# Kernel optimization log

Measured on AMD Instinct MI355X. Metric: run time of the kernel, lower is better.

The kernel has to match this reference:

```python
import jax, jax.numpy as jnp
import numpy as np

COMMITMENT_COST = 0.25


def setup_inputs() -> dict:
    key = jax.random.key(0)
    k1, k2 = jax.random.split(key)
    z_e = jax.random.normal(k1, (32, 256, 32, 32), dtype=jnp.float32)
    codebook = jax.random.normal(k2, (1024, 256), dtype=jnp.float32)
    return {"z_e": z_e, "codebook": codebook}


def reference(z_e, codebook):
    B, D, H, W = z_e.shape
    # (B, D, H, W) -> (N, D), N = B*H*W
    z_flat = jnp.transpose(z_e, (0, 2, 3, 1)).reshape(-1, D)
    # squared L2 distances to every codebook entry: (N, K)
    distances = (
        jnp.sum(z_flat * z_flat, axis=1, keepdims=True)
        - 2.0 * (z_flat @ codebook.T)
        + jnp.sum(codebook * codebook, axis=1)
    )
    codes = jnp.argmin(distances, axis=1)          # (N,)
    z_q = jnp.transpose(codebook[codes].reshape(B, H, W, D), (0, 3, 1, 2))
    # straight-through estimator
    z_q_st = z_e + jax.lax.stop_gradient(z_q - z_e)
    codebook_loss = jnp.mean((jax.lax.stop_gradient(z_q) - z_e) ** 2)
    commitment_loss = jnp.mean((z_q - jax.lax.stop_gradient(z_e)) ** 2)
    vq_loss = codebook_loss + COMMITMENT_COST * commitment_loss
    indices = codes.reshape(B, H, W)
    return z_q_st, indices, vq_loss
```

## Files before the change

kernel.cpp:

```cpp
#include <hip/hip_runtime.h>
#include <cstdint>
#include <cstddef>


typedef __attribute__((ext_vector_type(8))) short bf16x8;
typedef __attribute__((ext_vector_type(4))) float f32x4;

#define GL2LDS(g, l) __builtin_amdgcn_global_load_lds( \
    (__attribute__((address_space(1))) const void*)(g), \
    (__attribute__((address_space(3))) void*)(l), 16, 0, 0)

__device__ __forceinline__ unsigned short rne_bf16(float f) {
    unsigned u = __float_as_uint(f);
    return (unsigned short)((u + 0x7FFFu + ((u >> 16) & 1u)) >> 16);
}
__device__ __forceinline__ float bf16_to_f(unsigned short h) {
    return __uint_as_float((unsigned)h << 16);
}

__global__ __launch_bounds__(256)
void vq_cnorm_kernel(const float* __restrict__ cb, float* __restrict__ cnorm)
{
    const int k = blockIdx.x * 256 + threadIdx.x;
    const float4* row = reinterpret_cast<const float4*>(cb + (size_t)k * 256);
    float s0 = 0.f, s1 = 0.f, s2 = 0.f, s3 = 0.f;
#pragma unroll 8
    for (int i = 0; i < 64; ++i) {
        float4 v = row[i];
        s0 = fmaf(v.x, v.x, s0);
        s1 = fmaf(v.y, v.y, s1);
        s2 = fmaf(v.z, v.z, s2);
        s3 = fmaf(v.w, v.w, s3);
    }
    cnorm[k] = (s0 + s1) + (s2 + s3);
}

__global__ __launch_bounds__(256)
void vq_csplit_kernel(const float* __restrict__ cb, unsigned short* __restrict__ c0,
                      unsigned short* __restrict__ c1, unsigned short* __restrict__ c2)
{
    const int idx = blockIdx.x * 256 + threadIdx.x;
    float4 v = reinterpret_cast<const float4*>(cb)[idx];
    float f[4] = { v.x, v.y, v.z, v.w };
    ushort4 h0, h1, h2;
    unsigned short* p0[4] = { &h0.x, &h0.y, &h0.z, &h0.w };
    unsigned short* p1[4] = { &h1.x, &h1.y, &h1.z, &h1.w };
    unsigned short* p2[4] = { &h2.x, &h2.y, &h2.z, &h2.w };
#pragma unroll
    for (int j = 0; j < 4; ++j) {
        unsigned short b0 = rne_bf16(f[j]); float r1 = f[j] - bf16_to_f(b0);
        unsigned short b1 = rne_bf16(r1);   float r2 = r1 - bf16_to_f(b1);
        unsigned short b2 = rne_bf16(r2);
        *p0[j] = b0; *p1[j] = b1; *p2[j] = b2;
    }
    reinterpret_cast<ushort4*>(c0)[idx] = h0;
    reinterpret_cast<ushort4*>(c1)[idx] = h1;
    reinterpret_cast<ushort4*>(c2)[idx] = h2;
}

__global__ __launch_bounds__(256)
void vq_zsplit_kernel(const float* __restrict__ z, unsigned short* __restrict__ z0,
                      unsigned short* __restrict__ z1, unsigned short* __restrict__ z2)
{
    __shared__ float zl[64 * 264];
    const int t = threadIdx.x, blk = blockIdx.x;
    const int b = blk >> 4, hw0 = (blk & 15) << 6;
    const float* zb = z + ((size_t)b << 18) + hw0;
#pragma unroll 8
    for (int i = 0; i < 64; ++i) {
        int idx = i * 256 + t;
        int d = idx >> 6, hwl = idx & 63;
        zl[hwl * 264 + d] = zb[(size_t)d * 1024 + hwl];
    }
    __syncthreads();
    const int n0 = (b << 10) + hw0;
#pragma unroll
    for (int p = 0; p < 8; ++p) {
        const int hwl = p * 8 + (t >> 5);
        const int d0 = (t & 31) * 8;
        const float* src = &zl[hwl * 264 + d0];
        unsigned short h0[8], h1[8], h2[8];
#pragma unroll
        for (int j = 0; j < 8; ++j) {
            float f = src[j];
            unsigned short b0 = rne_bf16(f);  float r1 = f - bf16_to_f(b0);
            unsigned short b1 = rne_bf16(r1); float r2 = r1 - bf16_to_f(b1);
            unsigned short b2 = rne_bf16(r2);
            h0[j] = b0; h1[j] = b1; h2[j] = b2;
        }
        const size_t o = (size_t)(n0 + hwl) * 256 + d0;
        ushort4 a;
        a = ushort4{h0[0],h0[1],h0[2],h0[3]}; *reinterpret_cast<ushort4*>(z0 + o)     = a;
        a = ushort4{h0[4],h0[5],h0[6],h0[7]}; *reinterpret_cast<ushort4*>(z0 + o + 4) = a;
        a = ushort4{h1[0],h1[1],h1[2],h1[3]}; *reinterpret_cast<ushort4*>(z1 + o)     = a;
        a = ushort4{h1[4],h1[5],h1[6],h1[7]}; *reinterpret_cast<ushort4*>(z1 + o + 4) = a;
        a = ushort4{h2[0],h2[1],h2[2],h2[3]}; *reinterpret_cast<ushort4*>(z2 + o)     = a;
        a = ushort4{h2[4],h2[5],h2[6],h2[7]}; *reinterpret_cast<ushort4*>(z2 + o + 4) = a;
    }
}

__global__ __launch_bounds__(256)
void vq_mfma_argmin_kernel(const unsigned short* __restrict__ zp,
                           const unsigned short* __restrict__ cp,
                           const float* __restrict__ cnorm,
                           unsigned long long* __restrict__ packed)
{
    __shared__ unsigned short At[128 * 64];
    __shared__ unsigned short Bt[128 * 64];

    const int t = threadIdx.x, l = t & 63, w = t >> 6;
    const int wr = w >> 1, wc = w & 1;
    const int nid = ((blockIdx.x & 7) << 8) | (blockIdx.x >> 3);
    const int bm = nid >> 3, bn = nid & 7;
    const int arow = bm * 128, brow = bn * 128;

    const unsigned short* zparts[3] = { zp, zp + 8388608u, zp + 16777216u };
    const unsigned short* cparts[3] = { cp, cp + 262144u,  cp + 524288u };

    f32x4 acc[4][4];
#pragma unroll
    for (int m = 0; m < 4; ++m)
#pragma unroll
        for (int n = 0; n < 4; ++n) acc[m][n] = f32x4{0.f, 0.f, 0.f, 0.f};

    const int srow = w * 8 + (l >> 3);
    const int scol = (((l & 7) ^ ((l >> 3) & 7))) * 8;

    const int lo16 = l & 15, hi4 = l >> 4, l7 = l & 7;
    const int coff0 = ((hi4    ) ^ l7) * 8;
    const int coff1 = ((hi4 + 4) ^ l7) * 8;
    const unsigned short* Arow = &At[(wr * 64 + lo16) * 64];
    const unsigned short* Brow = &Bt[(wc * 64 + lo16) * 64];

    const int ASEG[6] = { 0, 1, 2, 0, 1, 0 };
    const int BSEG[6] = { 0, 0, 0, 1, 1, 2 };

#pragma unroll
    for (int seg = 0; seg < 6; ++seg) {
        const unsigned short* As = zparts[ASEG[seg]];
        const unsigned short* Bs = cparts[BSEG[seg]];
#pragma unroll
        for (int k4 = 0; k4 < 4; ++k4) {
            const int ko = k4 * 64;
            __syncthreads();
#pragma unroll
            for (int i = 0; i < 4; ++i) {
                GL2LDS(As + (size_t)(arow + i * 32 + srow) * 256 + ko + scol,
                       &At[(i * 32 + w * 8) * 64]);
                GL2LDS(Bs + (size_t)(brow + i * 32 + srow) * 256 + ko + scol,
                       &Bt[(i * 32 + w * 8) * 64]);
            }
            __syncthreads();
#pragma unroll
            for (int kk = 0; kk < 2; ++kk) {
                const int co = kk ? coff1 : coff0;
                bf16x8 a[4], b[4];
#pragma unroll
                for (int m = 0; m < 4; ++m)
                    a[m] = *reinterpret_cast<const bf16x8*>(Arow + m * 16 * 64 + co);
#pragma unroll
                for (int n = 0; n < 4; ++n)
                    b[n] = *reinterpret_cast<const bf16x8*>(Brow + n * 16 * 64 + co);
#pragma unroll
                for (int m = 0; m < 4; ++m)
#pragma unroll
                    for (int n = 0; n < 4; ++n)
                        acc[m][n] = __builtin_amdgcn_mfma_f32_16x16x32_bf16(
                            a[m], b[n], acc[m][n], 0, 0, 0);
            }
        }
    }

    int coln[4]; float cnv[4];
#pragma unroll
    for (int n = 0; n < 4; ++n) {
        coln[n] = brow + wc * 64 + n * 16 + (l & 15);
        cnv[n] = cnorm[coln[n]];
    }
#pragma unroll
    for (int m = 0; m < 4; ++m) {
#pragma unroll
        for (int j = 0; j < 4; ++j) {
            unsigned long long best = 0xFFFFFFFFFFFFFFFFull;
#pragma unroll
            for (int n = 0; n < 4; ++n) {
                float d = fmaf(-2.0f, acc[m][n][j], cnv[n]);
                unsigned u = __float_as_uint(d);
                u = (u & 0x80000000u) ? ~u : (u | 0x80000000u);
                unsigned long long pk = ((unsigned long long)u << 32) | (unsigned)coln[n];
                best = pk < best ? pk : best;
            }
#pragma unroll
            for (int mask = 1; mask <= 8; mask <<= 1) {
                unsigned long long o = __shfl_xor(best, mask, 64);
                best = o < best ? o : best;
            }
            if ((l & 15) == 0) {
                const int row = arow + wr * 64 + m * 16 + (l >> 4) * 4 + j;
                atomicMin(&packed[row], best);
            }
        }
    }
}

__global__ __launch_bounds__(256, 2)
void vq_gather_packed_kernel(const float* __restrict__ cb, const float* __restrict__ z,
                             const unsigned long long* __restrict__ packed,
                             float* __restrict__ out_zq, float* __restrict__ out_idx,
                             float* __restrict__ loss)
{
    __shared__ float rows[64 * 257];
    __shared__ int   ks[64];
    __shared__ float wsum[4];

    const int t   = threadIdx.x;
    const int blk = blockIdx.x;
    const int b   = blk >> 4;
    const int hw0 = (blk & 15) << 6;
    const int n0  = blk << 6;

    if (t < 64) {
        const int k = (int)(packed[n0 + t] & 0xFFFFFFFFull);
        ks[t] = k;
        out_idx[n0 + t] = (float)k;
    }
    __syncthreads();

#pragma unroll 4
    for (int i = 0; i < 64; ++i) {
        rows[i * 257 + t] = cb[(size_t)ks[i] * 256 + t];
    }
    __syncthreads();

    const int dq = t >> 6;
    const int hw = t & 63;
    const size_t obase = ((size_t)b << 18) + hw0 + hw;
    float sum = 0.f;
#pragma unroll 4
    for (int dd = 0; dd < 64; ++dd) {
        const int d = (dq << 6) + dd;
        const float  q  = rows[hw * 257 + d];
        const size_t a  = obase + (size_t)d * 1024;
        const float  zv = z[a];
        out_zq[a] = q;
        const float diff = q - zv;
        sum = fmaf(diff, diff, sum);
    }
#pragma unroll
    for (int m = 1; m <= 32; m <<= 1) sum += __shfl_xor(sum, m, 64);
    if ((t & 63) == 0) wsum[t >> 6] = sum;
    __syncthreads();
    if (t == 0) {
        const float s = (wsum[0] + wsum[1]) + (wsum[2] + wsum[3]);
        atomicAdd(loss, s * (1.25f / 8388608.0f));
    }
}

__global__ __launch_bounds__(256)
void vq_transpose_kernel(const float* __restrict__ cb, float* __restrict__ ctT)
{
    __shared__ float tile[64 * 65];
    const int t  = threadIdx.x;
    const int kb = blockIdx.x >> 2, db = blockIdx.x & 3;
    const int k0 = kb << 6, d0 = db << 6;
#pragma unroll
    for (int i = 0; i < 16; ++i) {
        int idx = i * 256 + t;
        int r = idx >> 6, c = idx & 63;
        tile[r * 65 + c] = cb[(size_t)(k0 + r) * 256 + d0 + c];
    }
    __syncthreads();
#pragma unroll
    for (int i = 0; i < 16; ++i) {
        int idx = i * 256 + t;
        int r = idx >> 6, c = idx & 63;
        ctT[(size_t)(d0 + r) * 1024 + k0 + c] = tile[c * 65 + r];
    }
}

__global__ __launch_bounds__(512, 2)
void vq_argmin_kernel(const float* __restrict__ z, const float* __restrict__ ctT,
                      const float* __restrict__ cnorm, int* __restrict__ codes,
                      float* __restrict__ out_idx)
{
    __shared__ float zt[256 * 64];
    __shared__ float ct[16 * 256];
    const int t = threadIdx.x, tx = t & 63, ty = t >> 6, p0 = ty << 3;
    const int blk = blockIdx.x, b = blk >> 4, hw0 = (blk & 15) << 6;
    const float* zbase = z + ((size_t)b << 18) + hw0;
#pragma unroll
    for (int i = 0; i < 8; ++i) {
        int idx = i * 512 + t;
        int d = idx >> 4, c4 = (idx & 15) << 2;
        float4 v = *reinterpret_cast<const float4*>(zbase + (size_t)d * 1024 + c4);
        *reinterpret_cast<float4*>(&zt[d * 64 + c4]) = v;
    }
    float minv[8]; int mini[8];
#pragma unroll
    for (int i = 0; i < 8; ++i) { minv[i] = 3.0e38f; mini[i] = 0; }
    const float* zrd = &zt[p0];
    const float* crd = &ct[tx << 2];
    for (int kt = 0; kt < 4; ++kt) {
        const int k0 = kt << 8;
        float acc[8][4];
#pragma unroll
        for (int i = 0; i < 8; ++i)
#pragma unroll
            for (int j = 0; j < 4; ++j) acc[i][j] = 0.f;
        for (int dc = 0; dc < 16; ++dc) {
            const int d0 = dc << 4;
            __syncthreads();
#pragma unroll
            for (int i = 0; i < 2; ++i) {
                int idx = i * 512 + t;
                int r = idx >> 6, c4 = (idx & 63) << 2;
                float4 v = *reinterpret_cast<const float4*>(ctT + (size_t)(d0 + r) * 1024 + k0 + c4);
                *reinterpret_cast<float4*>(&ct[r * 256 + c4]) = v;
            }
            __syncthreads();
            const float* zp = zrd + d0 * 64;
#pragma unroll
            for (int d = 0; d < 16; ++d) {
                float4 za = *reinterpret_cast<const float4*>(zp + d * 64);
                float4 zb = *reinterpret_cast<const float4*>(zp + d * 64 + 4);
                float4 cc = *reinterpret_cast<const float4*>(crd + d * 256);
#define VQ_FMA_ROW(ii, zv)                          \
                acc[ii][0] = fmaf(zv, cc.x, acc[ii][0]); \
                acc[ii][1] = fmaf(zv, cc.y, acc[ii][1]); \
                acc[ii][2] = fmaf(zv, cc.z, acc[ii][2]); \
                acc[ii][3] = fmaf(zv, cc.w, acc[ii][3]);
                VQ_FMA_ROW(0, za.x) VQ_FMA_ROW(1, za.y) VQ_FMA_ROW(2, za.z) VQ_FMA_ROW(3, za.w)
                VQ_FMA_ROW(4, zb.x) VQ_FMA_ROW(5, zb.y) VQ_FMA_ROW(6, zb.z) VQ_FMA_ROW(7, zb.w)
#undef VQ_FMA_ROW
            }
        }
#pragma unroll
        for (int j = 0; j < 4; ++j) {
            const int k = k0 + (tx << 2) + j;
            const float cn = cnorm[k];
#pragma unroll
            for (int i = 0; i < 8; ++i) {
                float dist = fmaf(-2.0f, acc[i][j], cn);
                if (dist < minv[i]) { minv[i] = dist; mini[i] = k; }
            }
        }
    }
#pragma unroll
    for (int m = 1; m <= 32; m <<= 1) {
#pragma unroll
        for (int i = 0; i < 8; ++i) {
            float ov = __shfl_xor(minv[i], m, 64);
            int   oi = __shfl_xor(mini[i], m, 64);
            if (ov < minv[i] || (ov == minv[i] && oi < mini[i])) { minv[i] = ov; mini[i] = oi; }
        }
    }
    if (tx == 0) {
        const int n0 = (blk << 6) + p0;
#pragma unroll
        for (int i = 0; i < 8; ++i) {
            codes[n0 + i]   = mini[i];
            out_idx[n0 + i] = (float)mini[i];
        }
    }
}

__global__ __launch_bounds__(256, 2)
void vq_gather_kernel(const float* __restrict__ cb, const float* __restrict__ z,
                      const int* __restrict__ codes, float* __restrict__ out_zq,
                      float* __restrict__ loss)
{
    __shared__ float rows[64 * 257];
    __shared__ int   ks[64];
    __shared__ float wsum[4];
    const int t = threadIdx.x, blk = blockIdx.x;
    const int b = blk >> 4, hw0 = (blk & 15) << 6, n0 = blk << 6;
    if (t < 64) ks[t] = codes[n0 + t];
    __syncthreads();
#pragma unroll 4
    for (int i = 0; i < 64; ++i) rows[i * 257 + t] = cb[(size_t)ks[i] * 256 + t];
    __syncthreads();
    const int dq = t >> 6, hw = t & 63;
    const size_t obase = ((size_t)b << 18) + hw0 + hw;
    float sum = 0.f;
#pragma unroll 4
    for (int dd = 0; dd < 64; ++dd) {
        const int d = (dq << 6) + dd;
        const float  q  = rows[hw * 257 + d];
        const size_t a  = obase + (size_t)d * 1024;
        const float  zv = z[a];
        out_zq[a] = q;
        const float diff = q - zv;
        sum = fmaf(diff, diff, sum);
    }
#pragma unroll
    for (int m = 1; m <= 32; m <<= 1) sum += __shfl_xor(sum, m, 64);
    if ((t & 63) == 0) wsum[t >> 6] = sum;
    __syncthreads();
    if (t == 0) {
        const float s = (wsum[0] + wsum[1]) + (wsum[2] + wsum[3]);
        atomicAdd(loss, s * (1.25f / 8388608.0f));
    }
}

extern "C" void kernel_launch(void* const* d_in, const int* in_sizes, int n_in,
                              void* d_out, int out_size, void* d_ws, size_t ws_size,
                              hipStream_t stream)
{
    (void)in_sizes; (void)n_in; (void)out_size;

    const float* z  = (const float*)d_in[0];
    const float* cb = (const float*)d_in[1];

    float* out      = (float*)d_out;
    float* out_zq   = out;
    float* out_idx  = out + 8388608;
    float* out_loss = out + 8421376;

    const size_t NEED = 262144ull + 3ull * 16777216ull + 3ull * 524288ull + 4096ull;

    if (ws_size >= NEED) {
        unsigned long long* packed = (unsigned long long*)d_ws;
        unsigned short* z0 = (unsigned short*)((char*)d_ws + 262144);
        unsigned short* z1 = z0 + 8388608u;
        unsigned short* z2 = z1 + 8388608u;
        unsigned short* c0 = z2 + 8388608u;
        unsigned short* c1 = c0 + 262144u;
        unsigned short* c2 = c1 + 262144u;
        float* cnorm = (float*)(c2 + 262144u);

        hipMemsetAsync(out_loss, 0, sizeof(float), stream);
        hipMemsetAsync(packed, 0xFF, 262144, stream);
        vq_csplit_kernel<<<256, 256, 0, stream>>>(cb, c0, c1, c2);
        vq_cnorm_kernel<<<4, 256, 0, stream>>>(cb, cnorm);
        vq_zsplit_kernel<<<512, 256, 0, stream>>>(z, z0, z1, z2);
        vq_mfma_argmin_kernel<<<2048, 256, 0, stream>>>(z0, c0, cnorm, packed);
        vq_gather_packed_kernel<<<512, 256, 0, stream>>>(cb, z, packed, out_zq, out_idx, out_loss);
    } else {
        float* ctT   = (float*)d_ws;
        float* cnorm = ctT + 256 * 1024;
        int*   codes = (int*)(cnorm + 1024);

        hipMemsetAsync(out_loss, 0, sizeof(float), stream);
        vq_transpose_kernel<<<64, 256, 0, stream>>>(cb, ctT);
        vq_cnorm_kernel<<<4, 256, 0, stream>>>(cb, cnorm);
        vq_argmin_kernel<<<512, 512, 0, stream>>>(z, ctT, cnorm, codes, out_idx);
        vq_gather_kernel<<<512, 256, 0, stream>>>(cb, z, codes, out_zq, out_loss);
    }
}
```

Before: 184.5 us.

## Triple-buffer LDS staging with 8-wave blocks in the MFMA argmin GEMM

Rewrites the bf16-split MFMA distance kernel to use 512 threads (8 waves, 2x4 layout) with a three-stage LDS ring. Global-to-LDS loads for stage s+2 are issued before computing stage s, and explicit vmcnt waits plus a single barrier per stage replace the two syncthreads per k-step. s_setprio is raised around the MFMA block. This is meant to hide global load latency behind MFMA work. In exchange it uses 96KB of LDS per block, which limits occupancy.

Result: slower. 285.0 us (+54.5%).

```diff
diff --git a/kernel.cpp b/kernel.cpp
--- a/kernel.cpp
+++ b/kernel.cpp
@@ -99,82 +99,97 @@
     }
 }
 
-__global__ __launch_bounds__(256)
+__global__ __launch_bounds__(512, 2)
 void vq_mfma_argmin_kernel(const unsigned short* __restrict__ zp,
                            const unsigned short* __restrict__ cp,
                            const float* __restrict__ cnorm,
                            unsigned long long* __restrict__ packed)
 {
-    __shared__ unsigned short At[128 * 64];
-    __shared__ unsigned short Bt[128 * 64];
+    __shared__ unsigned short Ld[3 * 16384];
 
     const int t = threadIdx.x, l = t & 63, w = t >> 6;
-    const int wr = w >> 1, wc = w & 1;
+    const int wr = w >> 2, wc = w & 3;
     const int nid = ((blockIdx.x & 7) << 8) | (blockIdx.x >> 3);
     const int bm = nid >> 3, bn = nid & 7;
     const int arow = bm * 128, brow = bn * 128;
 
-    const unsigned short* zparts[3] = { zp, zp + 8388608u, zp + 16777216u };
-    const unsigned short* cparts[3] = { cp, cp + 262144u,  cp + 524288u };
-
-    f32x4 acc[4][4];
+    f32x4 acc[4][2];
 #pragma unroll
     for (int m = 0; m < 4; ++m)
 #pragma unroll
-        for (int n = 0; n < 4; ++n) acc[m][n] = f32x4{0.f, 0.f, 0.f, 0.f};
-
-    const int srow = w * 8 + (l >> 3);
-    const int scol = (((l & 7) ^ ((l >> 3) & 7))) * 8;
+        for (int n = 0; n < 2; ++n) acc[m][n] = f32x4{0.f, 0.f, 0.f, 0.f};
+
+    const int srow = l >> 3;
+    const int scol = ((l & 7) ^ (l >> 3)) * 8;
 
     const int lo16 = l & 15, hi4 = l >> 4, l7 = l & 7;
     const int coff0 = ((hi4    ) ^ l7) * 8;
     const int coff1 = ((hi4 + 4) ^ l7) * 8;
-    const unsigned short* Arow = &At[(wr * 64 + lo16) * 64];
-    const unsigned short* Brow = &Bt[(wc * 64 + lo16) * 64];
-
-    const int ASEG[6] = { 0, 1, 2, 0, 1, 0 };
-    const int BSEG[6] = { 0, 0, 0, 1, 1, 2 };
-
-#pragma unroll
-    for (int seg = 0; seg < 6; ++seg) {
-        const unsigned short* As = zparts[ASEG[seg]];
-        const unsigned short* Bs = cparts[BSEG[seg]];
-#pragma unroll
-        for (int k4 = 0; k4 < 4; ++k4) {
-            const int ko = k4 * 64;
-            __syncthreads();
-#pragma unroll
-            for (int i = 0; i < 4; ++i) {
-                GL2LDS(As + (size_t)(arow + i * 32 + srow) * 256 + ko + scol,
-                       &At[(i * 32 + w * 8) * 64]);
-                GL2LDS(Bs + (size_t)(brow + i * 32 + srow) * 256 + ko + scol,
-                       &Bt[(i * 32 + w * 8) * 64]);
-            }
-            __syncthreads();
-#pragma unroll
-            for (int kk = 0; kk < 2; ++kk) {
-                const int co = kk ? coff1 : coff0;
-                bf16x8 a[4], b[4];
-#pragma unroll
-                for (int m = 0; m < 4; ++m)
-                    a[m] = *reinterpret_cast<const bf16x8*>(Arow + m * 16 * 64 + co);
-#pragma unroll
-                for (int n = 0; n < 4; ++n)
-                    b[n] = *reinterpret_cast<const bf16x8*>(Brow + n * 16 * 64 + co);
-#pragma unroll
-                for (int m = 0; m < 4; ++m)
-#pragma unroll
-                    for (int n = 0; n < 4; ++n)
-                        acc[m][n] = __builtin_amdgcn_mfma_f32_16x16x32_bf16(
-                            a[m], b[n], acc[m][n], 0, 0, 0);
-            }
-        }
-    }
-
-    int coln[4]; float cnv[4];
-#pragma unroll
-    for (int n = 0; n < 4; ++n) {
-        coln[n] = brow + wc * 64 + n * 16 + (l & 15);
+
+#define VQ_STAGE(ss, dstbase) do {                                            \
+    const int seg_ = (ss) >> 2, ko_ = ((ss) & 3) << 6;                        \
+    const unsigned short* As_ = zp + (size_t)((0x010210 >> (seg_ << 2)) & 3) * 8388608u; \
+    const unsigned short* Bs_ = cp + (size_t)((0x211000 >> (seg_ << 2)) & 3) * 262144u;  \
+    unsigned short* LA_ = (dstbase);                                          \
+    unsigned short* LB_ = (dstbase) + 8192;                                   \
+    GL2LDS(As_ + (size_t)(arow +      w * 8 + srow) * 256 + ko_ + scol, LA_ + (     w * 8) * 64); \
+    GL2LDS(As_ + (size_t)(arow + 64 + w * 8 + srow) * 256 + ko_ + scol, LA_ + (64 + w * 8) * 64); \
+    GL2LDS(Bs_ + (size_t)(brow +      w * 8 + srow) * 256 + ko_ + scol, LB_ + (     w * 8) * 64); \
+    GL2LDS(Bs_ + (size_t)(brow + 64 + w * 8 + srow) * 256 + ko_ + scol, LB_ + (64 + w * 8) * 64); \
+} while (0)
+
+    VQ_STAGE(0, Ld);
+    VQ_STAGE(1, Ld + 16384);
+    asm volatile("s_waitcnt vmcnt(4)" ::: "memory");
+    __builtin_amdgcn_sched_barrier(0);
+    __builtin_amdgcn_s_barrier();
+    __builtin_amdgcn_sched_barrier(0);
+
+    int cur = 0, stg = 2;
+    for (int s = 0; s < 24; ++s) {
+        if (s < 22) VQ_STAGE(s + 2, Ld + stg * 16384);
+
+        const unsigned short* LA = Ld + cur * 16384;
+        const unsigned short* LB = LA + 8192;
+        bf16x8 af[4][2], bf[2][2];
+#pragma unroll
+        for (int m = 0; m < 4; ++m) {
+            const unsigned short* r = &LA[(wr * 64 + m * 16 + lo16) * 64];
+            af[m][0] = *reinterpret_cast<const bf16x8*>(r + coff0);
+            af[m][1] = *reinterpret_cast<const bf16x8*>(r + coff1);
+        }
+#pragma unroll
+        for (int n = 0; n < 2; ++n) {
+            const unsigned short* r = &LB[(wc * 32 + n * 16 + lo16) * 64];
+            bf[n][0] = *reinterpret_cast<const bf16x8*>(r + coff0);
+            bf[n][1] = *reinterpret_cast<const bf16x8*>(r + coff1);
+        }
+        __builtin_amdgcn_s_setprio(1);
+#pragma unroll
+        for (int m = 0; m < 4; ++m)
+#pragma unroll
+            for (int n = 0; n < 2; ++n) {
+                acc[m][n] = __builtin_amdgcn_mfma_f32_16x16x32_bf16(af[m][0], bf[n][0], acc[m][n], 0, 0, 0);
+                acc[m][n] = __builtin_amdgcn_mfma_f32_16x16x32_bf16(af[m][1], bf[n][1], acc[m][n], 0, 0, 0);
+            }
+        __builtin_amdgcn_s_setprio(0);
+
+        if (s < 22)       { asm volatile("s_waitcnt vmcnt(4)" ::: "memory"); }
+        else if (s == 22) { asm volatile("s_waitcnt vmcnt(0)" ::: "memory"); }
+        __builtin_amdgcn_sched_barrier(0);
+        if (s < 23) {
+            __builtin_amdgcn_s_barrier();
+            __builtin_amdgcn_sched_barrier(0);
+        }
+        cur = (cur == 2) ? 0 : cur + 1;
+        stg = (stg == 2) ? 0 : stg + 1;
+    }
+#undef VQ_STAGE
+
+    int coln[2]; float cnv[2];
+#pragma unroll
+    for (int n = 0; n < 2; ++n) {
+        coln[n] = brow + wc * 32 + n * 16 + lo16;
         cnv[n] = cnorm[coln[n]];
     }
 #pragma unroll
@@ -183,7 +198,7 @@
         for (int j = 0; j < 4; ++j) {
             unsigned long long best = 0xFFFFFFFFFFFFFFFFull;
 #pragma unroll
-            for (int n = 0; n < 4; ++n) {
+            for (int n = 0; n < 2; ++n) {
                 float d = fmaf(-2.0f, acc[m][n][j], cnv[n]);
                 unsigned u = __float_as_uint(d);
                 u = (u & 0x80000000u) ? ~u : (u | 0x80000000u);
@@ -195,8 +210,8 @@
                 unsigned long long o = __shfl_xor(best, mask, 64);
                 best = o < best ? o : best;
             }
-            if ((l & 15) == 0) {
-                const int row = arow + wr * 64 + m * 16 + (l >> 4) * 4 + j;
+            if (lo16 == 0) {
+                const int row = arow + wr * 64 + m * 16 + hi4 * 4 + j;
                 atomicMin(&packed[row], best);
             }
         }
@@ -433,7 +448,7 @@
         vq_csplit_kernel<<<256, 256, 0, stream>>>(cb, c0, c1, c2);
         vq_cnorm_kernel<<<4, 256, 0, stream>>>(cb, cnorm);
         vq_zsplit_kernel<<<512, 256, 0, stream>>>(z, z0, z1, z2);
-        vq_mfma_argmin_kernel<<<2048, 256, 0, stream>>>(z0, c0, cnorm, packed);
+        vq_mfma_argmin_kernel<<<2048, 512, 0, stream>>>(z0, c0, cnorm, packed);
         vq_gather_packed_kernel<<<512, 256, 0, stream>>>(cb, z, packed, out_zq, out_idx, out_loss);
     } else {
         float* ctT   = (float*)d_ws;
```

## Double-buffer LDS tiles in MFMA argmin kernel to overlap loads with compute

Applied to the files above, without the earlier changes.

Gives the bf16 split-precision distance GEMM two LDS buffers for its A and B tiles. The global-to-LDS load for the next k-stage is issued before the MFMAs of the current stage, and the 6x4 segment loop is flattened into 24 stages. This removes one of the two barriers per stage and lets memory latency hide behind matrix math. LDS use per block doubles to 64 KB, which may cut the number of resident blocks per CU.

Measured after the change: 186.4 us. Within noise of the previous version (+1.0%).

```diff
diff --git a/kernel.cpp b/kernel.cpp
--- a/kernel.cpp
+++ b/kernel.cpp
@@ -105,8 +105,8 @@
                            const float* __restrict__ cnorm,
                            unsigned long long* __restrict__ packed)
 {
-    __shared__ unsigned short At[128 * 64];
-    __shared__ unsigned short Bt[128 * 64];
+    __shared__ unsigned short At[2][128 * 64];
+    __shared__ unsigned short Bt[2][128 * 64];
 
     const int t = threadIdx.x, l = t & 63, w = t >> 6;
     const int wr = w >> 1, wc = w & 1;
@@ -114,9 +114,6 @@
     const int bm = nid >> 3, bn = nid & 7;
     const int arow = bm * 128, brow = bn * 128;
 
-    const unsigned short* zparts[3] = { zp, zp + 8388608u, zp + 16777216u };
-    const unsigned short* cparts[3] = { cp, cp + 262144u,  cp + 524288u };
-
     f32x4 acc[4][4];
 #pragma unroll
     for (int m = 0; m < 4; ++m)
@@ -129,52 +126,59 @@
     const int lo16 = l & 15, hi4 = l >> 4, l7 = l & 7;
     const int coff0 = ((hi4    ) ^ l7) * 8;
     const int coff1 = ((hi4 + 4) ^ l7) * 8;
-    const unsigned short* Arow = &At[(wr * 64 + lo16) * 64];
-    const unsigned short* Brow = &Bt[(wc * 64 + lo16) * 64];
 
     const int ASEG[6] = { 0, 1, 2, 0, 1, 0 };
     const int BSEG[6] = { 0, 0, 0, 1, 1, 2 };
 
-#pragma unroll
-    for (int seg = 0; seg < 6; ++seg) {
-        const unsigned short* As = zparts[ASEG[seg]];
-        const unsigned short* Bs = cparts[BSEG[seg]];
-#pragma unroll
-        for (int k4 = 0; k4 < 4; ++k4) {
-            const int ko = k4 * 64;
-            __syncthreads();
-#pragma unroll
-            for (int i = 0; i < 4; ++i) {
-                GL2LDS(As + (size_t)(arow + i * 32 + srow) * 256 + ko + scol,
-                       &At[(i * 32 + w * 8) * 64]);
-                GL2LDS(Bs + (size_t)(brow + i * 32 + srow) * 256 + ko + scol,
-                       &Bt[(i * 32 + w * 8) * 64]);
-            }
-            __syncthreads();
-#pragma unroll
-            for (int kk = 0; kk < 2; ++kk) {
-                const int co = kk ? coff1 : coff0;
-                bf16x8 a[4], b[4];
-#pragma unroll
-                for (int m = 0; m < 4; ++m)
-                    a[m] = *reinterpret_cast<const bf16x8*>(Arow + m * 16 * 64 + co);
+#define VQ_STAGE(ss, bb) do {                                                 \
+    const unsigned short* As_ = zp + (size_t)ASEG[(ss) >> 2] * 8388608u;      \
+    const unsigned short* Bs_ = cp + (size_t)BSEG[(ss) >> 2] * 262144u;       \
+    const int ko_ = ((ss) & 3) << 6;                                          \
+    _Pragma("unroll")                                                         \
+    for (int i = 0; i < 4; ++i) {                                             \
+        GL2LDS(As_ + (size_t)(arow + i * 32 + srow) * 256 + ko_ + scol,       \
+               &At[bb][(i * 32 + w * 8) * 64]);                               \
+        GL2LDS(Bs_ + (size_t)(brow + i * 32 + srow) * 256 + ko_ + scol,       \
+               &Bt[bb][(i * 32 + w * 8) * 64]);                               \
+    }                                                                         \
+} while (0)
+
+    VQ_STAGE(0, 0);
+    __syncthreads();
+
+#pragma unroll
+    for (int s = 0; s < 24; ++s) {
+        const int cur = s & 1;
+        if (s < 23) VQ_STAGE(s + 1, cur ^ 1);
+        __builtin_amdgcn_sched_barrier(0);
+
+#pragma unroll
+        for (int kk = 0; kk < 2; ++kk) {
+            const int co = kk ? coff1 : coff0;
+            bf16x8 a[4], b[4];
+#pragma unroll
+            for (int m = 0; m < 4; ++m)
+                a[m] = *reinterpret_cast<const bf16x8*>(
+                    &At[cur][(wr * 64 + m * 16 + lo16) * 64 + co]);
+#pragma unroll
+            for (int n = 0; n < 4; ++n)
+                b[n] = *reinterpret_cast<const bf16x8*>(
+                    &Bt[cur][(wc * 64 + n * 16 + lo16) * 64 + co]);
+#pragma unroll
+            for (int m = 0; m < 4; ++m)
 #pragma unroll
                 for (int n = 0; n < 4; ++n)
-                    b[n] = *reinterpret_cast<const bf16x8*>(Brow + n * 16 * 64 + co);
-#pragma unroll
-                for (int m = 0; m < 4; ++m)
-#pragma unroll
-                    for (int n = 0; n < 4; ++n)
-                        acc[m][n] = __builtin_amdgcn_mfma_f32_16x16x32_bf16(
-                            a[m], b[n], acc[m][n], 0, 0, 0);
-            }
-        }
-    }
+                    acc[m][n] = __builtin_amdgcn_mfma_f32_16x16x32_bf16(
+                        a[m], b[n], acc[m][n], 0, 0, 0);
+        }
+        if (s < 23) __syncthreads();
+    }
+#undef VQ_STAGE
 
     int coln[4]; float cnv[4];
 #pragma unroll
     for (int n = 0; n < 4; ++n) {
-        coln[n] = brow + wc * 64 + n * 16 + (l & 15);
+        coln[n] = brow + wc * 64 + n * 16 + lo16;
         cnv[n] = cnorm[coln[n]];
     }
 #pragma unroll
@@ -195,8 +199,8 @@
                 unsigned long long o = __shfl_xor(best, mask, 64);
                 best = o < best ? o : best;
             }
-            if ((l & 15) == 0) {
-                const int row = arow + wr * 64 + m * 16 + (l >> 4) * 4 + j;
+            if (lo16 == 0) {
+                const int row = arow + wr * 64 + m * 16 + hi4 * 4 + j;
                 atomicMin(&packed[row], best);
             }
         }
```
